# Kernel tuning notes

Hardware: AMD Instinct MI355X
Metric: run time of the kernel (lower is better)

The kernel has to match this reference:

```python
import jax, jax.numpy as jnp
import numpy as np

D_MODEL = 2048
NUM_HEADS = 16
D_Q = 1536
D_KV = 512
BS, SL = 2, 2048


def _lin(x, w, b):
    # torch nn.Linear: y = x @ w.T + b, w: [out, in]
    return jnp.einsum('...i,oi->...o', x, w) + b


def _freqs(seq_len, dim, theta=10000.0):
    # Faithful to source incl. precedence quirk: tn = 1 / ((theta ** arange) / dim).
    # float32 overflow -> inf -> tn = 0 for large exponents (identity rotation).
    exps = jnp.arange(0, dim, 2, dtype=jnp.float32)
    tn = 1.0 / ((theta ** exps) / dim)
    m = jnp.arange(seq_len, dtype=jnp.float32)
    ang = jnp.outer(m, tn)  # [sl, dim/2]
    return jnp.cos(ang), jnp.sin(ang)


def _rope(x, cos, sin):
    # x: [bs, sl, dim]; complex pairs are (x[..., 2i], x[..., 2i+1])
    xe = x[..., 0::2]
    xo = x[..., 1::2]
    re = xe * cos - xo * sin
    im = xe * sin + xo * cos
    return jnp.stack([re, im], axis=-1).reshape(x.shape)


def _init_linear(key, out_f, in_f):
    k1, k2 = jax.random.split(key)
    bound = 1.0 / np.sqrt(in_f)
    w = jax.random.uniform(k1, (out_f, in_f), jnp.float32, -bound, bound)
    b = jax.random.uniform(k2, (out_f,), jnp.float32, -bound, bound)
    return w, b


def setup_inputs() -> dict:
    key = jax.random.key(0)
    ks = jax.random.split(key, 9)
    x = jax.random.normal(ks[0], (BS, SL, D_MODEL), jnp.float32)
    w_down_q, b_down_q = _init_linear(ks[1], D_Q, D_MODEL)
    w_up_q, b_up_q = _init_linear(ks[2], D_MODEL, D_Q)
    w_down_kv, b_down_kv = _init_linear(ks[3], D_KV, D_MODEL)
    w_up_k, b_up_k = _init_linear(ks[4], D_MODEL, D_KV)
    w_up_v, b_up_v = _init_linear(ks[5], D_MODEL, D_KV)
    wq_r, bq_r = _init_linear(ks[6], D_MODEL, D_Q)
    wk_r, bk_r = _init_linear(ks[7], D_MODEL, D_KV)
    wo, bo = _init_linear(ks[8], D_MODEL, D_MODEL)
    return dict(x=x,
                w_down_q=w_down_q, b_down_q=b_down_q,
                w_up_q=w_up_q, b_up_q=b_up_q,
                w_down_kv=w_down_kv, b_down_kv=b_down_kv,
                w_up_k=w_up_k, b_up_k=b_up_k,
                w_up_v=w_up_v, b_up_v=b_up_v,
                wq_r=wq_r, bq_r=bq_r,
                wk_r=wk_r, bk_r=bk_r,
                wo=wo, bo=bo)


def reference(x, w_down_q, b_down_q, w_up_q, b_up_q, w_down_kv, b_down_kv,
              w_up_k, b_up_k, w_up_v, b_up_v, wq_r, bq_r, wk_r, bk_r, wo, bo):
    bs, sl, dim = x.shape
    nh, hd = NUM_HEADS, dim // NUM_HEADS
    cos, sin = _freqs(sl, dim)

    # Query path: down-proj -> up-proj content + decoupled RoPE branch
    ct_q = _lin(x, w_down_q, b_down_q)                       # [bs, sl, d_q]
    q_ct = _lin(ct_q, w_up_q, b_up_q)                        # [bs, sl, d_model]
    rope_q = _rope(_lin(ct_q, wq_r, bq_r), cos, sin)         # [bs, sl, d_model]
    q = (q_ct + rope_q).reshape(bs, sl, nh, hd)

    # KV path: shared latent -> separate K/V up-proj + RoPE branch on K
    ct_kv = _lin(x, w_down_kv, b_down_kv)                    # [bs, sl, d_kv]
    k_ct = _lin(ct_kv, w_up_k, b_up_k)
    rope_k = _rope(_lin(ct_kv, wk_r, bk_r), cos, sin)
    k = (k_ct + rope_k).reshape(bs, sl, nh, hd)
    v = _lin(ct_kv, w_up_v, b_up_v).reshape(bs, sl, nh, hd)

    # Attention: explicit matmul + softmax + matmul (no causal mask in source)
    scores = jnp.einsum('bqhd,bkhd->bhqk', q, k) / np.sqrt(hd)
    probs = jax.nn.softmax(scores, axis=-1)
    a = jnp.einsum('bhqk,bkhd->bqhd', probs, v).reshape(bs, sl, nh * hd)
    return _lin(a, wo, bo)
```

## Files before the change

kernel.cpp:

```cpp
#include <hip/hip_runtime.h>

typedef float f32x4 __attribute__((ext_vector_type(4)));
typedef unsigned short us8 __attribute__((ext_vector_type(8)));

#define DEVINL __device__ __forceinline__

DEVINL unsigned short f2bf(float f) {
  unsigned u = __builtin_bit_cast(unsigned, f);
  u += 0x7fffu + ((u >> 16) & 1u);
  return (unsigned short)(u >> 16);
}
DEVINL float bf2f(unsigned short b) { return __builtin_bit_cast(float, ((unsigned)b) << 16); }
DEVINL us8 ld8(const unsigned short* p) { return *reinterpret_cast<const us8*>(p); }
DEVINL void mfma_bf16(f32x4& acc, us8 a, us8 b) {
  asm("v_mfma_f32_16x16x32_bf16 %0, %1, %2, %0" : "+v"(acc) : "v"(a), "v"(b));
}
DEVINL unsigned cvtpk_bf16(float lo, float hi) {
  unsigned r;
  asm("v_cvt_pk_bf16_f32 %0, %1, %2" : "=v"(r) : "v"(lo), "v"(hi));
  return r;
}
DEVINL void gld16(const void* g, void* l) {
  __builtin_amdgcn_global_load_lds((const __attribute__((address_space(1))) void*)g,
                                   (__attribute__((address_space(3))) void*)l, 16, 0, 0);
}

__global__ void k_cvt(const float* __restrict__ in, unsigned short* __restrict__ out, int n4) {
  int i = blockIdx.x * 256 + threadIdx.x;
  if (i >= n4) return;
  float4 v = reinterpret_cast<const float4*>(in)[i];
  unsigned lo = (unsigned)f2bf(v.x) | ((unsigned)f2bf(v.y) << 16);
  unsigned hi = (unsigned)f2bf(v.z) | ((unsigned)f2bf(v.w) << 16);
  reinterpret_cast<uint2*>(out)[i] = make_uint2(lo, hi);
}

__global__ void k_freqs(float* __restrict__ cosT, float* __restrict__ sinT) {
  int idx = blockIdx.x * 256 + threadIdx.x;
  if (idx >= 2048 * 1024) return;
  int s = idx >> 10, i = idx & 1023;
  float e = (float)(2 * i);
  float pw = powf(10000.0f, e);
  float tn = 1.0f / (pw / 2048.0f);
  float ang = (float)s * tn;
  cosT[idx] = cosf(ang);
  sinT[idx] = sinf(ang);
}

template <int BN, bool OUTF32>
__global__ __launch_bounds__(256) void k_gemm_bt(const unsigned short* __restrict__ A,
                                                 const unsigned short* __restrict__ B,
                                                 const float* __restrict__ bias,
                                                 void* __restrict__ Cout, int M, int N, int K,
                                                 int lda) {
  constexpr int NN = BN / 32;
  __shared__ unsigned short As[128 * 32];
  __shared__ unsigned short Bs[BN * 32];
  const int nwg = gridDim.x;
  const int q8 = nwg >> 3;
  const int orig = blockIdx.x;
  const int wgid = (orig & 7) * q8 + (orig >> 3);
  const int nbn = N / BN;
  const int bn = wgid % nbn, bm = wgid / nbn;
  const int tid = threadIdx.x, lane = tid & 63, w = tid >> 6;
  const int g = lane >> 4, l16 = lane & 15;
  const int wm = w >> 1, wn = w & 1;
  f32x4 acc[4][NN] = {};
  const unsigned short* Arow = A + (size_t)bm * 128 * lda;
  const unsigned short* Brow = B + (size_t)bn * BN * K;
  for (int kt = 0; kt < K; kt += 32) {
    __syncthreads();
#pragma unroll
    for (int j = 0; j < 2; ++j) {
      int c = (j * 4 + w) * 64 + lane;
      int row = c >> 2, c4 = c & 3;
      gld16(&Arow[(size_t)row * lda + kt + c4 * 8], &As[(j * 4 + w) * 512]);
    }
#pragma unroll
    for (int jb = 0; jb < BN / 64; ++jb) {
      int c = (jb * 4 + w) * 64 + lane;
      int row = c >> 2, c4 = c & 3;
      gld16(&Brow[(size_t)row * K + kt + c4 * 8], &Bs[(jb * 4 + w) * 512]);
    }
    __syncthreads();
    us8 af[4], bfg[NN];
#pragma unroll
    for (int mm = 0; mm < 4; ++mm) af[mm] = ld8(&As[(wm * 64 + mm * 16 + l16) * 32 + g * 8]);
#pragma unroll
    for (int nn = 0; nn < NN; ++nn)
      bfg[nn] = ld8(&Bs[(wn * (BN / 2) + nn * 16 + l16) * 32 + g * 8]);
#pragma unroll
    for (int mm = 0; mm < 4; ++mm)
#pragma unroll
      for (int nn = 0; nn < NN; ++nn) mfma_bf16(acc[mm][nn], af[mm], bfg[nn]);
  }
#pragma unroll
  for (int nn = 0; nn < NN; ++nn) {
    int col = bn * BN + wn * (BN / 2) + nn * 16 + l16;
    float bv = bias[col];
#pragma unroll
    for (int mm = 0; mm < 4; ++mm) {
      int row0 = bm * 128 + wm * 64 + mm * 16 + g * 4;
#pragma unroll
      for (int r = 0; r < 4; ++r) {
        float vv = acc[mm][nn][r] + bv;
        if (OUTF32)
          reinterpret_cast<float*>(Cout)[(size_t)(row0 + r) * N + col] = vv;
        else
          reinterpret_cast<unsigned short*>(Cout)[(size_t)(row0 + r) * N + col] = f2bf(vv);
      }
    }
  }
}

__global__ void k_rope_combine(const unsigned short* __restrict__ src, int ldin, float oscale,
                               const float* __restrict__ cosT, const float* __restrict__ sinT,
                               unsigned short* __restrict__ outp) {
  int pidx = blockIdx.x * 256 + threadIdx.x;
  if (pidx >= 4096 * 1024) return;
  int row = pidx >> 10, i = pidx & 1023;
  int s = row & 2047;
  float c = cosT[s * 1024 + i], sn = sinT[s * 1024 + i];
  const unsigned short* rp = src + (size_t)row * ldin;
  float xe = bf2f(rp[2048 + 2 * i]), xo = bf2f(rp[2048 + 2 * i + 1]);
  float re = xe * c - xo * sn;
  float im = xe * sn + xo * c;
  float q0 = (bf2f(rp[2 * i]) + re) * oscale;
  float q1 = (bf2f(rp[2 * i + 1]) + im) * oscale;
  unsigned pack = (unsigned)f2bf(q0) | ((unsigned)f2bf(q1) << 16);
  *reinterpret_cast<unsigned*>(&outp[(size_t)row * 2048 + 2 * i]) = pack;
}

__global__ __launch_bounds__(256) void k_transpose_v(const unsigned short* __restrict__ v, int ld,
                                                     unsigned short* __restrict__ vt) {
  __shared__ unsigned short t[32][33];
  int tx = threadIdx.x & 31, ty = threadIdx.x >> 5;
  int r0 = blockIdx.y * 32, c0 = blockIdx.x * 32;
#pragma unroll
  for (int jj = 0; jj < 4; ++jj)
    t[ty * 4 + jj][tx] = v[(size_t)(r0 + ty * 4 + jj) * ld + c0 + tx];
  __syncthreads();
  int b = r0 >> 11;
#pragma unroll
  for (int jj = 0; jj < 4; ++jj) {
    int colc = c0 + ty * 4 + jj;
    size_t orow = (size_t)(b * 16 + (colc >> 7)) * 128 + (colc & 127);
    vt[orow * 2048 + (r0 & 2047) + tx] = t[tx][ty * 4 + jj];
  }
}

__global__ __launch_bounds__(256, 2) void k_attn(const unsigned short* __restrict__ Q,
                                                 const unsigned short* __restrict__ Kg,
                                                 const unsigned short* __restrict__ VT,
                                                 unsigned short* __restrict__ Aout) {
  __shared__ unsigned short Ks[2][64 * 128];
  __shared__ unsigned short VTs[2][128 * 64];
  __shared__ unsigned short Ps[4][2][16 * 64];
  const int tid = threadIdx.x, lane = tid & 63, w = tid >> 6;
  const int g = lane >> 4, l16 = lane & 15;
  const int qt = blockIdx.x, h = blockIdx.y, b = blockIdx.z;
  us8 qf[2][4];
#pragma unroll
  for (int qg = 0; qg < 2; ++qg) {
    const size_t qrow = (size_t)b * 2048 + qt * 128 + w * 32 + qg * 16 + l16;
#pragma unroll
    for (int kc = 0; kc < 4; ++kc)
      qf[qg][kc] = ld8(&Q[qrow * 2048 + h * 128 + kc * 32 + g * 8]);
  }
  f32x4 O[2][8] = {};
  float mq[2] = {-1e30f, -1e30f}, lq[2] = {0.f, 0.f};
  const unsigned short* Kbase = Kg + (size_t)b * 2048 * 2048 + h * 128;
  const unsigned short* VTb = VT + (size_t)(b * 16 + h) * 128 * 2048;

  auto STAGE = [&](int bufi, int ktrow) {
#pragma unroll
    for (int j = 0; j < 4; ++j) {
      int ch = (j * 4 + w) * 64 + lane;
      int key = ch >> 4, cp = ch & 15;
      gld16(&Kbase[(size_t)(ktrow + key) * 2048 + (size_t)((cp ^ (key & 7)) * 8)],
            &Ks[bufi][(j * 4 + w) * 512]);
      int d = ch >> 3, c2 = ch & 7;
      gld16(&VTb[(size_t)d * 2048 + ktrow + (size_t)((c2 ^ (d & 7)) * 8)],
            &VTs[bufi][(j * 4 + w) * 512]);
    }
  };

  STAGE(0, 0);
  for (int t = 0; t < 32; ++t) {
    const int cur = t & 1;
    __syncthreads();
    if (t < 31) STAGE(cur ^ 1, (t + 1) * 64);
    const unsigned short* KsC = &Ks[cur][0];
    const unsigned short* VTsC = &VTs[cur][0];
    f32x4 st[2][4] = {};
    __builtin_amdgcn_s_setprio(1);
#pragma unroll
    for (int tt = 0; tt < 4; ++tt) {
      int key = tt * 16 + l16;
      int swz = (key & 7) << 3;
#pragma unroll
      for (int kc = 0; kc < 4; ++kc) {
        us8 kf = ld8(&KsC[key * 128 + ((kc * 32 + g * 8) ^ swz)]);
        mfma_bf16(st[0][tt], kf, qf[0][kc]);
        mfma_bf16(st[1][tt], kf, qf[1][kc]);
      }
    }
    __builtin_amdgcn_s_setprio(0);
    const int qswz = (l16 & 7) << 3;
#pragma unroll
    for (int qg = 0; qg < 2; ++qg) {
      float sv[16];
      float smax = -1e30f;
#pragma unroll
      for (int tt = 0; tt < 4; ++tt)
#pragma unroll
        for (int r = 0; r < 4; ++r) {
          sv[tt * 4 + r] = st[qg][tt][r];
          smax = fmaxf(smax, sv[tt * 4 + r]);
        }
      smax = fmaxf(smax, __shfl_xor(smax, 16));
      smax = fmaxf(smax, __shfl_xor(smax, 32));
      float mo = mq[qg];
      if (!__all(smax <= mo + 8.0f)) {
        float mn = fmaxf(mo, smax);
        float fac = exp2f(mo - mn);
        lq[qg] *= fac;
        mq[qg] = mn;
#pragma unroll
        for (int r = 0; r < 4; ++r) {
          float fr = __shfl(fac, g * 4 + r);
#pragma unroll
          for (int n0 = 0; n0 < 8; ++n0) O[qg][n0][r] *= fr;
        }
      }
      float mn = mq[qg];
      float ps = 0.f;
#pragma unroll
      for (int i = 0; i < 16; ++i) {
        sv[i] = exp2f(sv[i] - mn);
        ps += sv[i];
      }
      ps += __shfl_xor(ps, 16);
      ps += __shfl_xor(ps, 32);
      lq[qg] += ps;
      unsigned* P32 = reinterpret_cast<unsigned*>(&Ps[w][qg][0]);
#pragma unroll
      for (int tt = 0; tt < 4; ++tt)
#pragma unroll
        for (int pp = 0; pp < 2; ++pp) {
          int key = tt * 16 + g * 4 + pp * 2;
          unsigned pk = cvtpk_bf16(sv[tt * 4 + pp * 2], sv[tt * 4 + pp * 2 + 1]);
          int elem = l16 * 64 + (key ^ qswz);
          P32[elem >> 1] = pk;
        }
    }
    us8 pf[2][2];
#pragma unroll
    for (int qg = 0; qg < 2; ++qg)
#pragma unroll
      for (int kc = 0; kc < 2; ++kc)
        pf[qg][kc] = ld8(&Ps[w][qg][l16 * 64 + ((kc * 32 + g * 8) ^ qswz)]);
    __builtin_amdgcn_s_setprio(1);
#pragma unroll
    for (int n0 = 0; n0 < 8; ++n0) {
      int d = n0 * 16 + l16;
      int dsw = (d & 7) << 3;
#pragma unroll
      for (int kc = 0; kc < 2; ++kc) {
        us8 vf = ld8(&VTsC[d * 64 + ((kc * 32 + g * 8) ^ dsw)]);
        mfma_bf16(O[0][n0], pf[0][kc], vf);
        mfma_bf16(O[1][n0], pf[1][kc], vf);
      }
    }
    __builtin_amdgcn_s_setprio(0);
  }
#pragma unroll
  for (int qg = 0; qg < 2; ++qg) {
    float inv = 1.0f / lq[qg];
#pragma unroll
    for (int r = 0; r < 4; ++r) {
      float ir = __shfl(inv, g * 4 + r);
      size_t row = (size_t)b * 2048 + qt * 128 + w * 32 + qg * 16 + g * 4 + r;
#pragma unroll
      for (int n0 = 0; n0 < 8; ++n0)
        Aout[row * 2048 + h * 128 + n0 * 16 + l16] = f2bf(O[qg][n0][r] * ir);
    }
  }
}

extern "C" void kernel_launch(void* const* d_in, const int* in_sizes, int n_in, void* d_out,
                              int out_size, void* d_ws, size_t ws_size, hipStream_t stream) {
  (void)in_sizes; (void)n_in; (void)out_size; (void)ws_size;
  constexpr int Mr = 4096;
  using US = unsigned short;
  const float* x        = (const float*)d_in[0];
  const float* w_down_q = (const float*)d_in[1];
  const float* b_down_q = (const float*)d_in[2];
  const float* w_up_q   = (const float*)d_in[3];
  const float* b_up_q   = (const float*)d_in[4];
  const float* w_down_kv= (const float*)d_in[5];
  const float* b_down_kv= (const float*)d_in[6];
  const float* w_up_k   = (const float*)d_in[7];
  const float* b_up_k   = (const float*)d_in[8];
  const float* w_up_v   = (const float*)d_in[9];
  const float* b_up_v   = (const float*)d_in[10];
  const float* wq_r     = (const float*)d_in[11];
  const float* bq_r     = (const float*)d_in[12];
  const float* wk_r     = (const float*)d_in[13];
  const float* bk_r     = (const float*)d_in[14];
  const float* wo       = (const float*)d_in[15];
  const float* bo       = (const float*)d_in[16];

  char* p = (char*)d_ws;
  auto alloc = [&](size_t bytes) { char* r = p; p += (bytes + 255) & ~(size_t)255; return r; };
  float* cosT = (float*)alloc((size_t)2048 * 1024 * 4);
  float* sinT = (float*)alloc((size_t)2048 * 1024 * 4);
  US* xb        = (US*)alloc((size_t)Mr * 2048 * 2);
  US* wcat_down = (US*)alloc((size_t)2048 * 2048 * 2);
  US* wcat_qup  = (US*)alloc((size_t)4096 * 1536 * 2);
  US* wcat_kvup = (US*)alloc((size_t)6144 * 512 * 2);
  US* wob       = (US*)alloc((size_t)2048 * 2048 * 2);
  US* ct        = (US*)alloc((size_t)Mr * 2048 * 2);
  US* big       = (US*)alloc((size_t)Mr * 6144 * 2);
  US* vtb       = (US*)alloc((size_t)Mr * 2048 * 2);
  float* bcat_down = (float*)alloc(2048 * 4);
  float* bcat_qup  = (float*)alloc(4096 * 4);
  float* bcat_kvup = (float*)alloc(6144 * 4);
  US* qb   = xb;
  US* kb   = wcat_down;
  US* t12  = big;
  US* kv3  = big;
  US* aout = ct;

  auto cvt = [&](const float* s, US* dptr, size_t n) {
    int n4 = (int)(n / 4);
    k_cvt<<<dim3((n4 + 255) / 256), dim3(256), 0, stream>>>(s, dptr, n4);
  };
  cvt(x, xb, (size_t)Mr * 2048);
  cvt(w_down_q, wcat_down, (size_t)1536 * 2048);
  cvt(w_down_kv, wcat_down + (size_t)1536 * 2048, (size_t)512 * 2048);
  cvt(w_up_q, wcat_qup, (size_t)2048 * 1536);
  cvt(wq_r, wcat_qup + (size_t)2048 * 1536, (size_t)2048 * 1536);
  cvt(w_up_k, wcat_kvup, (size_t)2048 * 512);
  cvt(wk_r, wcat_kvup + (size_t)2048 * 512, (size_t)2048 * 512);
  cvt(w_up_v, wcat_kvup + (size_t)4096 * 512, (size_t)2048 * 512);
  cvt(wo, wob, (size_t)2048 * 2048);
  hipMemcpyAsync(bcat_down, b_down_q, 1536 * 4, hipMemcpyDeviceToDevice, stream);
  hipMemcpyAsync(bcat_down + 1536, b_down_kv, 512 * 4, hipMemcpyDeviceToDevice, stream);
  hipMemcpyAsync(bcat_qup, b_up_q, 2048 * 4, hipMemcpyDeviceToDevice, stream);
  hipMemcpyAsync(bcat_qup + 2048, bq_r, 2048 * 4, hipMemcpyDeviceToDevice, stream);
  hipMemcpyAsync(bcat_kvup, b_up_k, 2048 * 4, hipMemcpyDeviceToDevice, stream);
  hipMemcpyAsync(bcat_kvup + 2048, bk_r, 2048 * 4, hipMemcpyDeviceToDevice, stream);
  hipMemcpyAsync(bcat_kvup + 4096, b_up_v, 2048 * 4, hipMemcpyDeviceToDevice, stream);
  k_freqs<<<dim3((2048 * 1024 + 255) / 256), dim3(256), 0, stream>>>(cosT, sinT);

  const float SCQ = 0.08838834764831845f * 1.4426950408889634f;

  k_gemm_bt<64, false><<<dim3((2048 / 64) * (Mr / 128)), dim3(256), 0, stream>>>(
      xb, wcat_down, bcat_down, (void*)ct, Mr, 2048, 2048, 2048);
  k_gemm_bt<128, false><<<dim3((4096 / 128) * (Mr / 128)), dim3(256), 0, stream>>>(
      ct, wcat_qup, bcat_qup, (void*)t12, Mr, 4096, 1536, 2048);
  k_rope_combine<<<dim3((4096 * 1024 + 255) / 256), dim3(256), 0, stream>>>(t12, 4096, SCQ, cosT,
                                                                            sinT, qb);
  k_gemm_bt<128, false><<<dim3((6144 / 128) * (Mr / 128)), dim3(256), 0, stream>>>(
      ct + 1536, wcat_kvup, bcat_kvup, (void*)kv3, Mr, 6144, 512, 2048);
  k_rope_combine<<<dim3((4096 * 1024 + 255) / 256), dim3(256), 0, stream>>>(kv3, 6144, 1.0f, cosT,
                                                                            sinT, kb);
  k_transpose_v<<<dim3(64, 128), dim3(256), 0, stream>>>(kv3 + 4096, 6144, vtb);
  k_attn<<<dim3(16, 16, 2), dim3(256), 0, stream>>>(qb, kb, vtb, aout);
  k_gemm_bt<64, true><<<dim3((2048 / 64) * (Mr / 128)), dim3(256), 0, stream>>>(
      aout, wob, bo, d_out, Mr, 2048, 2048, 2048);
}
```

Baseline: 416.4 us.

## Fuse prep kernels and replace GEMM with triple-buffered 128x256 swizzled tile kernel

Merges the nine fp32-to-bf16 conversions, the RoPE frequency table and the bias concatenation into a single prep kernel, replacing many small launches and memcpys. Replaces the GEMM with a 512-thread, 128x256-tile kernel that uses a three-slot LDS ring buffer with asynchronous global-to-LDS loads, XOR-swizzled LDS layout to reduce bank conflicts, and raised wave priority around the MFMA block. The larger tiles give fewer workgroups, so some GEMMs may underfill the GPU's CUs. The deeper pipeline also raises LDS usage per workgroup.

```diff
diff --git a/kernel.cpp b/kernel.cpp
--- a/kernel.cpp
+++ b/kernel.cpp
@@ -25,84 +25,138 @@
                                    (__attribute__((address_space(3))) void*)l, 16, 0, 0);
 }
 
-__global__ void k_cvt(const float* __restrict__ in, unsigned short* __restrict__ out, int n4) {
-  int i = blockIdx.x * 256 + threadIdx.x;
-  if (i >= n4) return;
-  float4 v = reinterpret_cast<const float4*>(in)[i];
+DEVINL void cvt4(const float* __restrict__ s, unsigned short* __restrict__ d, long i) {
+  float4 v = reinterpret_cast<const float4*>(s)[i];
   unsigned lo = (unsigned)f2bf(v.x) | ((unsigned)f2bf(v.y) << 16);
   unsigned hi = (unsigned)f2bf(v.z) | ((unsigned)f2bf(v.w) << 16);
-  reinterpret_cast<uint2*>(out)[i] = make_uint2(lo, hi);
-}
-
-__global__ void k_freqs(float* __restrict__ cosT, float* __restrict__ sinT) {
-  int idx = blockIdx.x * 256 + threadIdx.x;
-  if (idx >= 2048 * 1024) return;
-  int s = idx >> 10, i = idx & 1023;
-  float e = (float)(2 * i);
-  float pw = powf(10000.0f, e);
-  float tn = 1.0f / (pw / 2048.0f);
-  float ang = (float)s * tn;
-  cosT[idx] = cosf(ang);
-  sinT[idx] = sinf(ang);
-}
-
-template <int BN, bool OUTF32>
-__global__ __launch_bounds__(256) void k_gemm_bt(const unsigned short* __restrict__ A,
+  reinterpret_cast<uint2*>(d)[i] = make_uint2(lo, hi);
+}
+
+__global__ void k_prep(const float* __restrict__ x, const float* __restrict__ wdq,
+                       const float* __restrict__ wdkv, const float* __restrict__ wuq,
+                       const float* __restrict__ wqr, const float* __restrict__ wuk,
+                       const float* __restrict__ wkr, const float* __restrict__ wuv,
+                       const float* __restrict__ wo, const float* __restrict__ bdq,
+                       const float* __restrict__ bdkv, const float* __restrict__ buq,
+                       const float* __restrict__ bqr, const float* __restrict__ buk,
+                       const float* __restrict__ bkr, const float* __restrict__ buv,
+                       unsigned short* __restrict__ xb, unsigned short* __restrict__ wcd,
+                       unsigned short* __restrict__ wcq, unsigned short* __restrict__ wck,
+                       unsigned short* __restrict__ wob, float* __restrict__ cosT,
+                       float* __restrict__ sinT, float* __restrict__ bcd,
+                       float* __restrict__ bcq, float* __restrict__ bck) {
+  constexpr long C0 = 2097152, C1 = C0 + 786432, C2 = C1 + 262144, C3 = C2 + 786432,
+                 C4 = C3 + 786432, C5 = C4 + 262144, C6 = C5 + 262144, C7 = C6 + 262144,
+                 C8 = C7 + 1048576, C9 = C8 + 2097152, C10 = C9 + 3072;
+  long u = (long)blockIdx.x * 256 + threadIdx.x;
+  if (u < C0) cvt4(x, xb, u);
+  else if (u < C1) cvt4(wdq, wcd, u - C0);
+  else if (u < C2) cvt4(wdkv, wcd + 1536L * 2048, u - C1);
+  else if (u < C3) cvt4(wuq, wcq, u - C2);
+  else if (u < C4) cvt4(wqr, wcq + 2048L * 1536, u - C3);
+  else if (u < C5) cvt4(wuk, wck, u - C4);
+  else if (u < C6) cvt4(wkr, wck + 2048L * 512, u - C5);
+  else if (u < C7) cvt4(wuv, wck + 4096L * 512, u - C6);
+  else if (u < C8) cvt4(wo, wob, u - C7);
+  else if (u < C9) {
+    long idx = u - C8;
+    int s = (int)(idx >> 10), i = (int)(idx & 1023);
+    float e = (float)(2 * i);
+    float pw = powf(10000.0f, e);
+    float tn = 1.0f / (pw / 2048.0f);
+    float ang = (float)s * tn;
+    cosT[idx] = cosf(ang);
+    sinT[idx] = sinf(ang);
+  } else if (u < C10) {
+    long j4 = (u - C9) * 4;
+#pragma unroll
+    for (int k = 0; k < 4; ++k) {
+      long j = j4 + k;
+      if (j < 2048) {
+        bcd[j] = j < 1536 ? bdq[j] : bdkv[j - 1536];
+      } else if (j < 6144) {
+        long jj = j - 2048;
+        bcq[jj] = jj < 2048 ? buq[jj] : bqr[jj - 2048];
+      } else {
+        long jj = j - 6144;
+        bck[jj] = jj < 2048 ? buk[jj] : (jj < 4096 ? bkr[jj - 2048] : buv[jj - 4096]);
+      }
+    }
+  }
+}
+
+template <bool OUTF32>
+__global__ __launch_bounds__(512) void k_gemm256(const unsigned short* __restrict__ A,
                                                  const unsigned short* __restrict__ B,
                                                  const float* __restrict__ bias,
-                                                 void* __restrict__ Cout, int M, int N, int K,
-                                                 int lda) {
-  constexpr int NN = BN / 32;
-  __shared__ unsigned short As[128 * 32];
-  __shared__ unsigned short Bs[BN * 32];
+                                                 void* __restrict__ Cout, int N, int K, int lda) {
+  constexpr int SLOT = 128 * 32 + 256 * 32;
+  __shared__ unsigned short lds[3 * SLOT];
   const int nwg = gridDim.x;
-  const int q8 = nwg >> 3;
   const int orig = blockIdx.x;
-  const int wgid = (orig & 7) * q8 + (orig >> 3);
-  const int nbn = N / BN;
+  const int wgid = (orig & 7) * (nwg >> 3) + (orig >> 3);
+  const int nbn = N >> 8;
   const int bn = wgid % nbn, bm = wgid / nbn;
   const int tid = threadIdx.x, lane = tid & 63, w = tid >> 6;
   const int g = lane >> 4, l16 = lane & 15;
-  const int wm = w >> 1, wn = w & 1;
-  f32x4 acc[4][NN] = {};
-  const unsigned short* Arow = A + (size_t)bm * 128 * lda;
-  const unsigned short* Brow = B + (size_t)bn * BN * K;
-  for (int kt = 0; kt < K; kt += 32) {
-    __syncthreads();
-#pragma unroll
-    for (int j = 0; j < 2; ++j) {
-      int c = (j * 4 + w) * 64 + lane;
-      int row = c >> 2, c4 = c & 3;
-      gld16(&Arow[(size_t)row * lda + kt + c4 * 8], &As[(j * 4 + w) * 512]);
-    }
-#pragma unroll
-    for (int jb = 0; jb < BN / 64; ++jb) {
-      int c = (jb * 4 + w) * 64 + lane;
-      int row = c >> 2, c4 = c & 3;
-      gld16(&Brow[(size_t)row * K + kt + c4 * 8], &Bs[(jb * 4 + w) * 512]);
-    }
-    __syncthreads();
-    us8 af[4], bfg[NN];
-#pragma unroll
-    for (int mm = 0; mm < 4; ++mm) af[mm] = ld8(&As[(wm * 64 + mm * 16 + l16) * 32 + g * 8]);
-#pragma unroll
-    for (int nn = 0; nn < NN; ++nn)
-      bfg[nn] = ld8(&Bs[(wn * (BN / 2) + nn * 16 + l16) * 32 + g * 8]);
-#pragma unroll
-    for (int mm = 0; mm < 4; ++mm)
-#pragma unroll
-      for (int nn = 0; nn < NN; ++nn) mfma_bf16(acc[mm][nn], af[mm], bfg[nn]);
-  }
-#pragma unroll
-  for (int nn = 0; nn < NN; ++nn) {
-    int col = bn * BN + wn * (BN / 2) + nn * 16 + l16;
+  const int wm = w >> 2, wn = w & 3;
+  f32x4 acc[4][4] = {};
+  const unsigned short* Abase = A + (size_t)bm * 128 * lda;
+  const unsigned short* Bbase = B + (size_t)bn * 256 * K;
+  const int ra = tid >> 2;
+  const int gca = (tid & 3) ^ ((ra >> 1) & 3);
+  const int rb1 = (tid + 512) >> 2;
+  const int gcb1 = ((tid + 512) & 3) ^ ((rb1 >> 1) & 3);
+  const size_t aoff = (size_t)ra * lda + gca * 8;
+  const size_t boff0 = (size_t)ra * K + gca * 8;
+  const size_t boff1 = (size_t)rb1 * K + gcb1 * 8;
+  auto STAGE = [&](int slot, int kt) {
+    unsigned short* s = &lds[slot * SLOT];
+    gld16(Abase + aoff + kt, s + tid * 8);
+    gld16(Bbase + boff0 + kt, s + 128 * 32 + tid * 8);
+    gld16(Bbase + boff1 + kt, s + 128 * 32 + (tid + 512) * 8);
+  };
+  const int nt = K >> 5;
+  STAGE(0, 0);
+  STAGE(1, 32);
+  asm volatile("s_waitcnt vmcnt(3)" ::: "memory");
+  asm volatile("s_barrier" ::: "memory");
+  for (int t = 0; t < nt; ++t) {
+    const int slot = t % 3;
+    if (t + 2 < nt) STAGE((t + 2) % 3, (t + 2) * 32);
+    const unsigned short* sa = &lds[slot * SLOT];
+    const unsigned short* sb = sa + 128 * 32;
+    us8 af[4], bf[4];
+#pragma unroll
+    for (int m = 0; m < 4; ++m) {
+      int row = wm * 64 + m * 16 + l16;
+      af[m] = ld8(&sa[row * 32 + ((g ^ ((row >> 1) & 3)) * 8)]);
+    }
+#pragma unroll
+    for (int n = 0; n < 4; ++n) {
+      int row = wn * 64 + n * 16 + l16;
+      bf[n] = ld8(&sb[row * 32 + ((g ^ ((row >> 1) & 3)) * 8)]);
+    }
+    __builtin_amdgcn_s_setprio(1);
+#pragma unroll
+    for (int m = 0; m < 4; ++m)
+#pragma unroll
+      for (int n = 0; n < 4; ++n) mfma_bf16(acc[m][n], af[m], bf[n]);
+    __builtin_amdgcn_s_setprio(0);
+    if (t < nt - 2) asm volatile("s_waitcnt vmcnt(3)" ::: "memory");
+    else            asm volatile("s_waitcnt vmcnt(0)" ::: "memory");
+    asm volatile("s_barrier" ::: "memory");
+  }
+#pragma unroll
+  for (int n = 0; n < 4; ++n) {
+    int col = bn * 256 + wn * 64 + n * 16 + l16;
     float bv = bias[col];
 #pragma unroll
-    for (int mm = 0; mm < 4; ++mm) {
-      int row0 = bm * 128 + wm * 64 + mm * 16 + g * 4;
+    for (int m = 0; m < 4; ++m) {
+      int row0 = bm * 128 + wm * 64 + m * 16 + g * 4;
 #pragma unroll
       for (int r = 0; r < 4; ++r) {
-        float vv = acc[mm][nn][r] + bv;
+        float vv = acc[m][n][r] + bv;
         if (OUTF32)
           reinterpret_cast<float*>(Cout)[(size_t)(row0 + r) * N + col] = vv;
         else
@@ -331,42 +385,25 @@
   US* kv3  = big;
   US* aout = ct;
 
-  auto cvt = [&](const float* s, US* dptr, size_t n) {
-    int n4 = (int)(n / 4);
-    k_cvt<<<dim3((n4 + 255) / 256), dim3(256), 0, stream>>>(s, dptr, n4);
-  };
-  cvt(x, xb, (size_t)Mr * 2048);
-  cvt(w_down_q, wcat_down, (size_t)1536 * 2048);
-  cvt(w_down_kv, wcat_down + (size_t)1536 * 2048, (size_t)512 * 2048);
-  cvt(w_up_q, wcat_qup, (size_t)2048 * 1536);
-  cvt(wq_r, wcat_qup + (size_t)2048 * 1536, (size_t)2048 * 1536);
-  cvt(w_up_k, wcat_kvup, (size_t)2048 * 512);
-  cvt(wk_r, wcat_kvup + (size_t)2048 * 512, (size_t)2048 * 512);
-  cvt(w_up_v, wcat_kvup + (size_t)4096 * 512, (size_t)2048 * 512);
-  cvt(wo, wob, (size_t)2048 * 2048);
-  hipMemcpyAsync(bcat_down, b_down_q, 1536 * 4, hipMemcpyDeviceToDevice, stream);
-  hipMemcpyAsync(bcat_down + 1536, b_down_kv, 512 * 4, hipMemcpyDeviceToDevice, stream);
-  hipMemcpyAsync(bcat_qup, b_up_q, 2048 * 4, hipMemcpyDeviceToDevice, stream);
-  hipMemcpyAsync(bcat_qup + 2048, bq_r, 2048 * 4, hipMemcpyDeviceToDevice, stream);
-  hipMemcpyAsync(bcat_kvup, b_up_k, 2048 * 4, hipMemcpyDeviceToDevice, stream);
-  hipMemcpyAsync(bcat_kvup + 2048, bk_r, 2048 * 4, hipMemcpyDeviceToDevice, stream);
-  hipMemcpyAsync(bcat_kvup + 4096, b_up_v, 2048 * 4, hipMemcpyDeviceToDevice, stream);
-  k_freqs<<<dim3((2048 * 1024 + 255) / 256), dim3(256), 0, stream>>>(cosT, sinT);
+  k_prep<<<dim3(33804), dim3(256), 0, stream>>>(
+      x, w_down_q, w_down_kv, w_up_q, wq_r, w_up_k, wk_r, w_up_v, wo, b_down_q, b_down_kv,
+      b_up_q, bq_r, b_up_k, bk_r, b_up_v, xb, wcat_down, wcat_qup, wcat_kvup, wob, cosT, sinT,
+      bcat_down, bcat_qup, bcat_kvup);
 
   const float SCQ = 0.08838834764831845f * 1.4426950408889634f;
 
-  k_gemm_bt<64, false><<<dim3((2048 / 64) * (Mr / 128)), dim3(256), 0, stream>>>(
-      xb, wcat_down, bcat_down, (void*)ct, Mr, 2048, 2048, 2048);
-  k_gemm_bt<128, false><<<dim3((4096 / 128) * (Mr / 128)), dim3(256), 0, stream>>>(
-      ct, wcat_qup, bcat_qup, (void*)t12, Mr, 4096, 1536, 2048);
+  k_gemm256<false><<<dim3((2048 / 256) * (Mr / 128)), dim3(512), 0, stream>>>(
+      xb, wcat_down, bcat_down, (void*)ct, 2048, 2048, 2048);
+  k_gemm256<false><<<dim3((4096 / 256) * (Mr / 128)), dim3(512), 0, stream>>>(
+      ct, wcat_qup, bcat_qup, (void*)t12, 4096, 1536, 2048);
   k_rope_combine<<<dim3((4096 * 1024 + 255) / 256), dim3(256), 0, stream>>>(t12, 4096, SCQ, cosT,
                                                                             sinT, qb);
-  k_gemm_bt<128, false><<<dim3((6144 / 128) * (Mr / 128)), dim3(256), 0, stream>>>(
-      ct + 1536, wcat_kvup, bcat_kvup, (void*)kv3, Mr, 6144, 512, 2048);
+  k_gemm256<false><<<dim3((6144 / 256) * (Mr / 128)), dim3(512), 0, stream>>>(
+      ct + 1536, wcat_kvup, bcat_kvup, (void*)kv3, 6144, 512, 2048);
   k_rope_combine<<<dim3((4096 * 1024 + 255) / 256), dim3(256), 0, stream>>>(kv3, 6144, 1.0f, cosT,
                                                                             sinT, kb);
   k_transpose_v<<<dim3(64, 128), dim3(256), 0, stream>>>(kv3 + 4096, 6144, vtb);
   k_attn<<<dim3(16, 16, 2), dim3(256), 0, stream>>>(qb, kb, vtb, aout);
-  k_gemm_bt<64, true><<<dim3((2048 / 64) * (Mr / 128)), dim3(256), 0, stream>>>(
-      aout, wob, bo, d_out, Mr, 2048, 2048, 2048);
-}
+  k_gemm256<true><<<dim3((2048 / 256) * (Mr / 128)), dim3(512), 0, stream>>>(
+      aout, wob, bo, d_out, 2048, 2048, 2048);
+}
```

Measured after the change: 362.8 us. 12.9% less time.
